# Kernel optimization log

Hardware: AMD Instinct MI355X
Metric: run time of the kernel (lower is better)

## Reference

```python
import jax, jax.numpy as jnp
import numpy as np

H = 300          # hidden_size
M = 256          # molecules
L = 128          # atoms per molecule (uniform -> pad/unpad is a reshape)
A = 1 + M * L    # atoms incl. zero-padding row 0
NB = 6           # max neighbor bonds per atom
B = 1 + 4 * M * L  # directed bonds incl. zero-padding row 0
ATOM_FDIM = 133
BOND_FDIM = 147
DEPTH = 3


def _lin(key, out_d, in_d):
    return (jax.random.normal(key, (out_d, in_d), jnp.float32) / np.sqrt(in_d)).astype(jnp.float32)


def setup_inputs() -> dict:
    key = jax.random.key(0)
    ks = jax.random.split(key, 24)
    s = 1.0 / np.sqrt(H)
    return {
        "f_atoms": jax.random.normal(ks[0], (A, ATOM_FDIM), jnp.float32),
        "f_bonds": jax.random.normal(ks[1], (B, BOND_FDIM), jnp.float32),
        "a2b": jax.random.randint(ks[2], (A, NB), 0, B),
        "b2a": jax.random.randint(ks[3], (B,), 0, A),
        "b2revb": jax.random.randint(ks[4], (B,), 0, B),
        "W_i_atom": _lin(ks[5], H, ATOM_FDIM),
        "W_i_bond": _lin(ks[6], H, BOND_FDIM),
        "W_h0": _lin(ks[7], H, H),
        "W_h1": _lin(ks[8], H, H),
        "W_lr": _lin(ks[9], H, 3 * H),
        "gru_bias": jax.random.uniform(ks[10], (H,), jnp.float32, -s, s),
        "Wih_f": _lin(ks[11], 3 * H, H),
        "Whh_f": _lin(ks[12], 3 * H, H),
        "bih_f": jax.random.uniform(ks[13], (3 * H,), jnp.float32, -s, s),
        "bhh_f": jax.random.uniform(ks[14], (3 * H,), jnp.float32, -s, s),
        "Wih_b": _lin(ks[15], 3 * H, H),
        "Whh_b": _lin(ks[16], 3 * H, H),
        "bih_b": jax.random.uniform(ks[17], (3 * H,), jnp.float32, -s, s),
        "bhh_b": jax.random.uniform(ks[18], (3 * H,), jnp.float32, -s, s),
        "W_o": _lin(ks[19], H, 2 * H),
        "b_o": jax.random.uniform(ks[20], (H,), jnp.float32, -s, s),
    }


def _gru_dir(x, h0, Wih, Whh, bih, bhh, reverse):
    # x: [M, T, H], h0: [M, H] -> outputs [M, T, H], torch.nn.GRU gate math
    gi_all = jnp.swapaxes(x, 0, 1) @ Wih.T + bih  # [T, M, 3H]

    def step(h, gi):
        gh = h @ Whh.T + bhh
        ir, iz, inn = jnp.split(gi, 3, axis=-1)
        hr, hz, hn = jnp.split(gh, 3, axis=-1)
        r = jax.nn.sigmoid(ir + hr)
        z = jax.nn.sigmoid(iz + hz)
        n = jnp.tanh(inn + r * hn)
        h_new = (1.0 - z) * n + z * h
        return h_new, h_new

    _, ys = jax.lax.scan(step, h0, gi_all, reverse=reverse)
    return jnp.swapaxes(ys, 0, 1)


def reference(f_atoms, f_bonds, a2b, b2a, b2revb, W_i_atom, W_i_bond, W_h0, W_h1,
              W_lr, gru_bias, Wih_f, Whh_f, bih_f, bhh_f, Wih_b, Whh_b, bih_b, bhh_b,
              W_o, b_o):
    relu = jax.nn.relu
    input_atom = relu(f_atoms @ W_i_atom.T)            # [A, H]
    message_atom = input_atom
    input_bond = relu(f_bonds @ W_i_bond.T)            # [B, H]
    message_bond = input_bond

    W_h = [W_h0, W_h1]
    for d in range(DEPTH - 1):
        nei = message_bond[a2b]                        # [A, NB, H] gather
        agg = nei.sum(axis=1) * nei.max(axis=1)        # sum * max aggregation
        message_atom = message_atom + agg
        rev = message_bond[b2revb]                     # [B, H]
        message_bond = message_atom[b2a] - rev
        message_bond = message_bond @ W_h[d].T
        message_bond = relu(input_bond + message_bond)  # dropout p=0

    nei = message_bond[a2b]
    agg = nei.sum(axis=1) * nei.max(axis=1)
    node = jnp.concatenate([agg, message_atom, input_atom], axis=1) @ W_lr.T  # [A, H]

    # BatchGRU: uniform molecule sizes -> pad/unpad is a reshape
    message = relu(node + gru_bias)                    # [A, H]
    msg = message[1:].reshape(M, L, H)
    hid = node[1:].reshape(M, L, H)
    h0 = hid.max(axis=1)                               # [M, H] per-mol max init state
    out_f = _gru_dir(msg, h0, Wih_f, Whh_f, bih_f, bhh_f, reverse=False)
    out_b = _gru_dir(msg, h0, Wih_b, Whh_b, bih_b, bhh_b, reverse=True)
    gru_out = jnp.concatenate([out_f, out_b], axis=-1).reshape(M * L, 2 * H)
    row0 = jnp.concatenate([message[0:1], message[0:1]], axis=1)
    agg2 = jnp.concatenate([row0, gru_out], axis=0)    # [A, 2H]

    atom_hiddens = relu(agg2 @ W_o.T + b_o)            # [A, H]
    mol_vecs = atom_hiddens[1:].reshape(M, L, H).mean(axis=1)  # [M, H]
    return mol_vecs
```

## Files before the change

kernel.cpp:

```cpp
#include <hip/hip_runtime.h>
#include <math.h>

#define HH   300
#define H3   900
#define MMOL 256
#define LATM 128
#define AA   32769
#define NBB  6
#define BBND 131073
#define AFD  133
#define BFD  147
#define MLR  (MMOL * LATM)

static __device__ __forceinline__ float sigm(float x) { return 1.0f / (1.0f + expf(-x)); }

template<bool RELU, bool BIAS, bool ACCUM>
__global__ __launch_bounds__(256)
void gemm_big(const float* __restrict__ X, int ldx, const float* __restrict__ W, int ldw,
              const float* __restrict__ Bias, float* __restrict__ C,
              int rows, int N, int K)
{
    __shared__ float Xs[16][132];
    __shared__ float Ws[16][68];
    const int row0 = blockIdx.x * 128;
    const int col0 = blockIdx.y * 64;
    const int tid  = threadIdx.x;
    const int tm   = (tid >> 4) * 8;
    const int tn   = (tid & 15) * 4;
    const bool xv  = ((ldx & 3) == 0);
    const bool wv  = ((ldw & 3) == 0);

    float acc[8][4];
#pragma unroll
    for (int i = 0; i < 8; ++i)
#pragma unroll
        for (int j = 0; j < 4; ++j) acc[i][j] = 0.0f;

    for (int k0 = 0; k0 < K; k0 += 16) {
        const int rem = K - k0;
#pragma unroll
        for (int l = 0; l < 2; ++l) {
            int s = tid + l * 256;
            int r = s >> 2, kq = (s & 3) * 4;
            int gr = row0 + r;
            float v0 = 0, v1 = 0, v2 = 0, v3 = 0;
            if (gr < rows) {
                const float* xp = X + (long)gr * ldx + k0 + kq;
                if (xv && rem >= 16) {
                    float4 t4 = *(const float4*)xp;
                    v0 = t4.x; v1 = t4.y; v2 = t4.z; v3 = t4.w;
                } else {
                    if (kq + 0 < rem) v0 = xp[0];
                    if (kq + 1 < rem) v1 = xp[1];
                    if (kq + 2 < rem) v2 = xp[2];
                    if (kq + 3 < rem) v3 = xp[3];
                }
            }
            Xs[kq + 0][r] = v0; Xs[kq + 1][r] = v1;
            Xs[kq + 2][r] = v2; Xs[kq + 3][r] = v3;
        }
        {
            int r = tid >> 2, kq = (tid & 3) * 4;
            int gc = col0 + r;
            float v0 = 0, v1 = 0, v2 = 0, v3 = 0;
            if (gc < N) {
                const float* wp = W + (long)gc * ldw + k0 + kq;
                if (wv && rem >= 16) {
                    float4 t4 = *(const float4*)wp;
                    v0 = t4.x; v1 = t4.y; v2 = t4.z; v3 = t4.w;
                } else {
                    if (kq + 0 < rem) v0 = wp[0];
                    if (kq + 1 < rem) v1 = wp[1];
                    if (kq + 2 < rem) v2 = wp[2];
                    if (kq + 3 < rem) v3 = wp[3];
                }
            }
            Ws[kq + 0][r] = v0; Ws[kq + 1][r] = v1;
            Ws[kq + 2][r] = v2; Ws[kq + 3][r] = v3;
        }
        __syncthreads();
#pragma unroll
        for (int kk = 0; kk < 16; ++kk) {
            float4 xa = *(const float4*)&Xs[kk][tm];
            float4 xb = *(const float4*)&Xs[kk][tm + 4];
            float4 wq = *(const float4*)&Ws[kk][tn];
            float xr[8] = {xa.x, xa.y, xa.z, xa.w, xb.x, xb.y, xb.z, xb.w};
            float wr[4] = {wq.x, wq.y, wq.z, wq.w};
#pragma unroll
            for (int i = 0; i < 8; ++i)
#pragma unroll
                for (int j = 0; j < 4; ++j)
                    acc[i][j] += xr[i] * wr[j];
        }
        __syncthreads();
    }

#pragma unroll
    for (int i = 0; i < 8; ++i) {
        int gr = row0 + tm + i;
        if (gr >= rows) continue;
#pragma unroll
        for (int j = 0; j < 4; ++j) {
            int gc = col0 + tn + j;
            if (gc >= N) continue;
            float v = acc[i][j];
            if (BIAS)  v += Bias[gc];
            if (ACCUM) v += C[(long)gr * N + gc];
            if (RELU)  v = fmaxf(v, 0.0f);
            C[(long)gr * N + gc] = v;
        }
    }
}

__global__ void transpose_kernel(const float* __restrict__ in, float* __restrict__ out,
                                 int N, int K)
{
    long idx = (long)blockIdx.x * blockDim.x + threadIdx.x;
    if (idx >= (long)N * K) return;
    int k = (int)(idx / N), n = (int)(idx - (long)k * N);
    out[idx] = in[(long)n * K + k];
}

__global__ __launch_bounds__(256)
void vw_hi_gemm(float* __restrict__ P, const float* __restrict__ W, int rows)
{
    __shared__ float Xs[16][132];
    __shared__ float Ws[16][192];
    const int row0 = blockIdx.x * 128;
    const int tid  = threadIdx.x;
    const int tm   = (tid >> 4) * 8;
    const int tn   = (tid & 15) * 4;

    float acc[8][12];
#pragma unroll
    for (int i = 0; i < 8; ++i)
#pragma unroll
        for (int j = 0; j < 12; ++j) acc[i][j] = 0.0f;

    for (int k0 = 0; k0 < 300; k0 += 16) {
        const int rem = 300 - k0;
#pragma unroll
        for (int l = 0; l < 2; ++l) {
            int s = tid + l * 256;
            int r = s >> 2, kq = (s & 3) * 4;
            int gr = row0 + r;
            float v0 = 0, v1 = 0, v2 = 0, v3 = 0;
            if (gr < rows) {
                const float* xp = P + (long)gr * 300 + k0 + kq;
                if (rem >= 16) {
                    float4 t4 = *(const float4*)xp;
                    v0 = t4.x; v1 = t4.y; v2 = t4.z; v3 = t4.w;
                } else {
                    if (kq + 0 < rem) v0 = xp[0];
                    if (kq + 1 < rem) v1 = xp[1];
                    if (kq + 2 < rem) v2 = xp[2];
                    if (kq + 3 < rem) v3 = xp[3];
                }
            }
            Xs[kq + 0][r] = v0; Xs[kq + 1][r] = v1;
            Xs[kq + 2][r] = v2; Xs[kq + 3][r] = v3;
        }
        for (int s = tid; s < 600; s += 256) {
            int r = s >> 2, kq = (s & 3) * 4;
            const float* wp = W + (long)(150 + r) * 300 + k0 + kq;
            float v0 = 0, v1 = 0, v2 = 0, v3 = 0;
            if (rem >= 16) {
                float4 t4 = *(const float4*)wp;
                v0 = t4.x; v1 = t4.y; v2 = t4.z; v3 = t4.w;
            } else {
                if (kq + 0 < rem) v0 = wp[0];
                if (kq + 1 < rem) v1 = wp[1];
                if (kq + 2 < rem) v2 = wp[2];
                if (kq + 3 < rem) v3 = wp[3];
            }
            Ws[kq + 0][r] = v0; Ws[kq + 1][r] = v1;
            Ws[kq + 2][r] = v2; Ws[kq + 3][r] = v3;
        }
        __syncthreads();
#pragma unroll
        for (int kk = 0; kk < 16; ++kk) {
            float4 xa = *(const float4*)&Xs[kk][tm];
            float4 xb = *(const float4*)&Xs[kk][tm + 4];
            float4 w0 = *(const float4*)&Ws[kk][tn];
            float4 w1 = *(const float4*)&Ws[kk][tn + 64];
            float4 w2 = *(const float4*)&Ws[kk][tn + 128];
            float xr[8] = {xa.x, xa.y, xa.z, xa.w, xb.x, xb.y, xb.z, xb.w};
            float wr[12] = {w0.x, w0.y, w0.z, w0.w, w1.x, w1.y, w1.z, w1.w,
                            w2.x, w2.y, w2.z, w2.w};
#pragma unroll
            for (int i = 0; i < 8; ++i)
#pragma unroll
                for (int j = 0; j < 12; ++j)
                    acc[i][j] += xr[i] * wr[j];
        }
        __syncthreads();
    }

#pragma unroll
    for (int i = 0; i < 8; ++i) {
        int gr = row0 + tm + i;
        if (gr >= rows) continue;
#pragma unroll
        for (int c = 0; c < 3; ++c)
#pragma unroll
            for (int j = 0; j < 4; ++j) {
                int cn = tn + c * 64 + j;
                if (cn < 150) P[(long)gr * 300 + cn] = acc[i][c * 4 + j];
            }
    }
}

__global__ __launch_bounds__(256)
void bond_half(const float* __restrict__ FB, const float* __restrict__ WiB,
               const float* __restrict__ Th, const float* __restrict__ Vsrc, int vstride,
               const int* __restrict__ b2a, const int* __restrict__ b2revb,
               float* __restrict__ P, int c0, int rows)
{
    __shared__ float Xs[16][132];
    __shared__ float Ws[16][68];
    __shared__ int ra[128], rb[128];
    const int row0 = blockIdx.x * 128;
    const int col0 = blockIdx.y * 64;
    const int tid  = threadIdx.x;

    if (tid < 128) {
        int gr = row0 + tid;
        ra[tid] = (gr < rows) ? b2a[gr] : 0;
    } else {
        int m = tid - 128;
        int gr = row0 + m;
        rb[m] = (gr < rows) ? b2revb[gr] : 0;
    }

    const int tm = (tid >> 4) * 8;
    const int tn = (tid & 15) * 4;
    float acc[8][4];
#pragma unroll
    for (int i = 0; i < 8; ++i)
#pragma unroll
        for (int j = 0; j < 4; ++j) acc[i][j] = 0.0f;

    for (int k0 = 0; k0 < BFD; k0 += 16) {
        const int rem = BFD - k0;
#pragma unroll
        for (int l = 0; l < 2; ++l) {
            int s = tid + l * 256;
            int r = s >> 2, kq = (s & 3) * 4;
            int gr = row0 + r;
            float v0 = 0, v1 = 0, v2 = 0, v3 = 0;
            if (gr < rows) {
                const float* xp = FB + (long)gr * BFD + k0 + kq;
                if (kq + 0 < rem) v0 = xp[0];
                if (kq + 1 < rem) v1 = xp[1];
                if (kq + 2 < rem) v2 = xp[2];
                if (kq + 3 < rem) v3 = xp[3];
            }
            Xs[kq + 0][r] = v0; Xs[kq + 1][r] = v1;
            Xs[kq + 2][r] = v2; Xs[kq + 3][r] = v3;
        }
        {
            int r = tid >> 2, kq = (tid & 3) * 4;
            int gc = col0 + r;
            float v0 = 0, v1 = 0, v2 = 0, v3 = 0;
            if (gc < 150) {
                const float* wp = WiB + (long)(c0 + gc) * BFD + k0 + kq;
                if (kq + 0 < rem) v0 = wp[0];
                if (kq + 1 < rem) v1 = wp[1];
                if (kq + 2 < rem) v2 = wp[2];
                if (kq + 3 < rem) v3 = wp[3];
            }
            Ws[kq + 0][r] = v0; Ws[kq + 1][r] = v1;
            Ws[kq + 2][r] = v2; Ws[kq + 3][r] = v3;
        }
        __syncthreads();
#pragma unroll
        for (int kk = 0; kk < 16; ++kk) {
            float4 xa = *(const float4*)&Xs[kk][tm];
            float4 xb = *(const float4*)&Xs[kk][tm + 4];
            float4 wq = *(const float4*)&Ws[kk][tn];
            float xr[8] = {xa.x, xa.y, xa.z, xa.w, xb.x, xb.y, xb.z, xb.w};
            float wr[4] = {wq.x, wq.y, wq.z, wq.w};
#pragma unroll
            for (int i = 0; i < 8; ++i)
#pragma unroll
                for (int j = 0; j < 4; ++j)
                    acc[i][j] += xr[i] * wr[j];
        }
        __syncthreads();
    }

#pragma unroll
    for (int i = 0; i < 8; ++i) {
        int gr = row0 + tm + i;
        if (gr >= rows) continue;
        int a  = ra[tm + i];
        int rv = rb[tm + i];
#pragma unroll
        for (int j = 0; j < 4; ++j) {
            int cn = col0 + tn + j;
            if (cn >= 150) continue;
            float ib = fmaxf(acc[i][j], 0.0f);
            float v  = ib + Th[(long)a * 150 + cn] - Vsrc[(long)rv * vstride + cn];
            P[(long)gr * 300 + c0 + cn] = fmaxf(v, 0.0f);
        }
    }
}

template<bool ADD>
__global__ void aggregate(const float* __restrict__ mb, const int* __restrict__ a2b,
                          float* __restrict__ dst)
{
    long idx = (long)blockIdx.x * blockDim.x + threadIdx.x;
    if (idx >= (long)AA * HH) return;
    int a = (int)(idx / HH);
    int h = (int)(idx - (long)a * HH);
    const int* nb = a2b + (long)a * NBB;
    float s = 0.0f, mx = -INFINITY;
#pragma unroll
    for (int i = 0; i < NBB; ++i) {
        float v = mb[(long)nb[i] * HH + h];
        s += v;
        mx = fmaxf(mx, v);
    }
    float r = s * mx;
    if (ADD) r += dst[idx];
    dst[idx] = r;
}

__global__ void msgx_kernel(const float* __restrict__ node, const float* __restrict__ gbias,
                            float* __restrict__ msgx)
{
    long idx = (long)blockIdx.x * blockDim.x + threadIdx.x;
    if (idx >= (long)MLR * HH) return;
    int h = (int)(idx % HH);
    msgx[idx] = fmaxf(node[idx + HH] + gbias[h], 0.0f);
}

__global__ void h0_kernel(const float* __restrict__ node, float* __restrict__ hf)
{
    int idx = blockIdx.x * blockDim.x + threadIdx.x;
    if (idx >= MMOL * HH) return;
    int m = idx / HH;
    int h = idx - m * HH;
    long base = (long)(1 + m * LATM) * HH + h;
    float mx = -INFINITY;
    for (int t = 0; t < LATM; ++t) mx = fmaxf(mx, node[base + (long)t * HH]);
    hf[idx] = mx;
}

__global__ __launch_bounds__(1024)
void gru_scan3(const float* __restrict__ WhhT_f, const float* __restrict__ bhh_f,
               const float* __restrict__ WhhT_b, const float* __restrict__ bhh_b,
               const float* __restrict__ h0, float* __restrict__ gi_f,
               float* __restrict__ gi_b)
{
    const int bid  = blockIdx.x;
    const int xcd  = bid & 7;
    const int dir  = (xcd >= 4) ? 1 : 0;
    const int rank = (bid >> 3) * 4 + (xcd & 3);
    const int m0   = rank * 2;
    const float* WhhT = dir ? WhhT_b : WhhT_f;
    const float* bhh  = dir ? bhh_b  : bhh_f;
    float*       gi   = dir ? gi_b   : gi_f;
    const int tid = threadIdx.x;

    __shared__ float hs[2][304];
    __shared__ float ghs[2][H3];

    float bb = (tid < H3) ? bhh[tid] : 0.0f;

    for (int i = tid; i < 150; i += 1024) {
        int mm = i / 75, q = (i - mm * 75) * 4;
        *(float4*)&hs[mm][q] = *(const float4*)&h0[(long)(m0 + mm) * HH + q];
    }
    __syncthreads();

    for (int s = 0; s < LATM; ++s) {
        const int t = dir ? (LATM - 1 - s) : s;

        if (tid < H3) {
            float a0 = 0.0f, a1 = 0.0f;
            const float* wh = WhhT + tid;
#pragma unroll 4
            for (int k0 = 0; k0 < HH; k0 += 4) {
                float w0 = wh[(long)(k0 + 0) * H3];
                float w1 = wh[(long)(k0 + 1) * H3];
                float w2 = wh[(long)(k0 + 2) * H3];
                float w3 = wh[(long)(k0 + 3) * H3];
                float4 h0v = *(const float4*)&hs[0][k0];
                float4 h1v = *(const float4*)&hs[1][k0];
                a0 += h0v.x * w0 + h0v.y * w1 + h0v.z * w2 + h0v.w * w3;
                a1 += h1v.x * w0 + h1v.y * w1 + h1v.z * w2 + h1v.w * w3;
            }
            ghs[0][tid] = a0 + bb;
            ghs[1][tid] = a1 + bb;
        }
        __syncthreads();

        if (tid < 2 * HH) {
            int mm = tid / HH, hh = tid - mm * HH;
            long row = (long)(m0 + mm) * LATM + t;
            float* g = gi + row * H3;
            float ir = g[hh], iz = g[HH + hh], inn = g[2 * HH + hh];
            float r  = sigm(ir + ghs[mm][hh]);
            float z  = sigm(iz + ghs[mm][HH + hh]);
            float nn = tanhf(inn + r * ghs[mm][2 * HH + hh]);
            float hn = (1.0f - z) * nn + z * hs[mm][hh];
            hs[mm][hh] = hn;
            g[hh] = hn;
        }
        __syncthreads();
    }
}

__global__ void mean_kernel(const float* __restrict__ ah, float* __restrict__ out)
{
    int idx = blockIdx.x * blockDim.x + threadIdx.x;
    if (idx >= MMOL * HH) return;
    int m = idx / HH;
    int j = idx - m * HH;
    long base = (long)m * LATM * HH + j;
    float s = 0.0f;
    for (int t = 0; t < LATM; ++t) s += ah[base + (long)t * HH];
    out[idx] = s * (1.0f / LATM);
}

static inline int cdiv(long a, long b) { return (int)((a + b - 1) / b); }

extern "C" void kernel_launch(void* const* d_in, const int* in_sizes, int n_in,
                              void* d_out, int out_size, void* d_ws, size_t ws_size,
                              hipStream_t stream)
{
    const float* f_atoms  = (const float*)d_in[0];
    const float* f_bonds  = (const float*)d_in[1];
    const int*   a2b      = (const int*)d_in[2];
    const int*   b2a      = (const int*)d_in[3];
    const int*   b2revb   = (const int*)d_in[4];
    const float* W_i_atom = (const float*)d_in[5];
    const float* W_i_bond = (const float*)d_in[6];
    const float* W_h0     = (const float*)d_in[7];
    const float* W_h1     = (const float*)d_in[8];
    const float* W_lr     = (const float*)d_in[9];
    const float* gru_bias = (const float*)d_in[10];
    const float* Wih_f    = (const float*)d_in[11];
    const float* Whh_f    = (const float*)d_in[12];
    const float* bih_f    = (const float*)d_in[13];
    const float* bhh_f    = (const float*)d_in[14];
    const float* Wih_b    = (const float*)d_in[15];
    const float* Whh_b    = (const float*)d_in[16];
    const float* bih_b    = (const float*)d_in[17];
    const float* bhh_b    = (const float*)d_in[18];
    const float* W_o      = (const float*)d_in[19];
    const float* b_o      = (const float*)d_in[20];
    float* out = (float*)d_out;

    const size_t NEED = 295530016;
    if (ws_size < NEED) return;

    char* b = (char*)d_ws;
    float* P   = (float*)b;
    float* S   = (float*)(b + 157287600);
    float* MA  = (float*)(b + 235931408);
    float* TH  = (float*)(b + 275254208);

    float* Pia  = P + (size_t)AA * HH;
    float* giF  = (float*)b;
    float* giB  = (float*)(b + 117964800);
    float* MSGX = MA;
    float* AH   = MA;
    float* H0   = TH;
    float* WhhT_f = TH + 76800;
    float* WhhT_b = TH + 346800;

    dim3 blk(256);
    const int gA = cdiv((long)AA * HH, 256);
    dim3 gmA (cdiv(AA, 128),   cdiv(HH, 64));
    dim3 gmB3(cdiv(BBND, 128), cdiv(HH, 64));
    dim3 gmB1(cdiv(BBND, 128), cdiv(150, 64));
    dim3 gmT (cdiv(AA, 128),   cdiv(150, 64));
    dim3 gmG (cdiv(MLR, 128),  cdiv(H3, 64));
    dim3 gmO (cdiv(MLR, 128),  cdiv(HH, 64));

    gemm_big<true, false, false><<<gmA, blk, 0, stream>>>(
        f_atoms, AFD, W_i_atom, AFD, nullptr, MA, AA, HH, AFD);
    gemm_big<true, false, false><<<gmB3, blk, 0, stream>>>(
        f_bonds, BFD, W_i_bond, BFD, nullptr, P, BBND, HH, BFD);

    const float* Wh[2] = { W_h0, W_h1 };
    for (int d = 0; d < 2; ++d) {
        const float* W = Wh[d];
        aggregate<true><<<gA, blk, 0, stream>>>(P, a2b, MA);
        gemm_big<false, false, false><<<gmB1, blk, 0, stream>>>(
            P, HH, W, HH, nullptr, S, BBND, 150, HH);
        vw_hi_gemm<<<cdiv(BBND, 128), blk, 0, stream>>>(P, W, BBND);
        gemm_big<false, false, false><<<gmT, blk, 0, stream>>>(
            MA, HH, W + 150 * HH, HH, nullptr, TH, AA, 150, HH);
        bond_half<<<gmB1, blk, 0, stream>>>(
            f_bonds, W_i_bond, TH, P, 300, b2a, b2revb, P, 150, BBND);
        gemm_big<false, false, false><<<gmT, blk, 0, stream>>>(
            MA, HH, W, HH, nullptr, TH, AA, 150, HH);
        bond_half<<<gmB1, blk, 0, stream>>>(
            f_bonds, W_i_bond, TH, S, 150, b2a, b2revb, P, 0, BBND);
    }

    aggregate<false><<<gA, blk, 0, stream>>>(P, a2b, S);

    gemm_big<true, false, false><<<gmA, blk, 0, stream>>>(
        f_atoms, AFD, W_i_atom, AFD, nullptr, Pia, AA, HH, AFD);
    gemm_big<false, false, false><<<gmA, blk, 0, stream>>>(
        S,   HH, W_lr,          H3, nullptr, P, AA, HH, HH);
    gemm_big<false, false, true><<<gmA, blk, 0, stream>>>(
        MA,  HH, W_lr + HH,     H3, nullptr, P, AA, HH, HH);
    gemm_big<false, false, true><<<gmA, blk, 0, stream>>>(
        Pia, HH, W_lr + 2 * HH, H3, nullptr, P, AA, HH, HH);

    msgx_kernel<<<cdiv((long)MLR * HH, 256), blk, 0, stream>>>(P, gru_bias, MSGX);
    h0_kernel<<<cdiv(MMOL * HH, 256), blk, 0, stream>>>(P, H0);
    transpose_kernel<<<cdiv(270000, 256), blk, 0, stream>>>(Whh_f, WhhT_f, H3, HH);
    transpose_kernel<<<cdiv(270000, 256), blk, 0, stream>>>(Whh_b, WhhT_b, H3, HH);

    gemm_big<false, true, false><<<gmG, blk, 0, stream>>>(
        MSGX, HH, Wih_f, HH, bih_f, giF, MLR, H3, HH);
    gemm_big<false, true, false><<<gmG, blk, 0, stream>>>(
        MSGX, HH, Wih_b, HH, bih_b, giB, MLR, H3, HH);

    gru_scan3<<<dim3(256), dim3(1024), 0, stream>>>(
        WhhT_f, bhh_f, WhhT_b, bhh_b, H0, giF, giB);

    gemm_big<false, false, false><<<gmO, blk, 0, stream>>>(
        giF, H3, W_o,      2 * HH, nullptr, AH, MLR, HH, HH);
    gemm_big<true, true, true><<<gmO, blk, 0, stream>>>(
        giB, H3, W_o + HH, 2 * HH, b_o,     AH, MLR, HH, HH);

    mean_kernel<<<cdiv(MMOL * HH, 256), blk, 0, stream>>>(AH, out);
}
```

Before: 5.624 ms.

## Register-prefetch next GEMM tile and vectorize GRU recurrent weight loads

The generic tiled GEMM now loads the next K-tile from global memory into registers while the current shared-memory tile is being computed, so load latency overlaps with FMA work. Separately, the recurrent weights Whh are repacked into groups of four consecutive k-values per output, so the GRU scan can fetch them with one float4 load instead of four strided scalar loads. The prefetch costs extra registers in the GEMM and may lower occupancy, and the repack kernel hardcodes the 900x300 shape.

```diff
diff --git a/kernel.cpp b/kernel.cpp
--- a/kernel.cpp
+++ b/kernel.cpp
@@ -30,13 +30,9 @@
     const bool xv  = ((ldx & 3) == 0);
     const bool wv  = ((ldw & 3) == 0);
 
-    float acc[8][4];
-#pragma unroll
-    for (int i = 0; i < 8; ++i)
-#pragma unroll
-        for (int j = 0; j < 4; ++j) acc[i][j] = 0.0f;
-
-    for (int k0 = 0; k0 < K; k0 += 16) {
+    float px[2][4], pw[4];
+
+    auto loadTile = [&](int k0) {
         const int rem = K - k0;
 #pragma unroll
         for (int l = 0; l < 2; ++l) {
@@ -56,8 +52,7 @@
                     if (kq + 3 < rem) v3 = xp[3];
                 }
             }
-            Xs[kq + 0][r] = v0; Xs[kq + 1][r] = v1;
-            Xs[kq + 2][r] = v2; Xs[kq + 3][r] = v3;
+            px[l][0] = v0; px[l][1] = v1; px[l][2] = v2; px[l][3] = v3;
         }
         {
             int r = tid >> 2, kq = (tid & 3) * 4;
@@ -75,10 +70,35 @@
                     if (kq + 3 < rem) v3 = wp[3];
                 }
             }
-            Ws[kq + 0][r] = v0; Ws[kq + 1][r] = v1;
-            Ws[kq + 2][r] = v2; Ws[kq + 3][r] = v3;
-        }
-        __syncthreads();
+            pw[0] = v0; pw[1] = v1; pw[2] = v2; pw[3] = v3;
+        }
+    };
+    auto commitTile = [&]() {
+#pragma unroll
+        for (int l = 0; l < 2; ++l) {
+            int s = tid + l * 256;
+            int r = s >> 2, kq = (s & 3) * 4;
+            Xs[kq + 0][r] = px[l][0]; Xs[kq + 1][r] = px[l][1];
+            Xs[kq + 2][r] = px[l][2]; Xs[kq + 3][r] = px[l][3];
+        }
+        {
+            int r = tid >> 2, kq = (tid & 3) * 4;
+            Ws[kq + 0][r] = pw[0]; Ws[kq + 1][r] = pw[1];
+            Ws[kq + 2][r] = pw[2]; Ws[kq + 3][r] = pw[3];
+        }
+    };
+
+    float acc[8][4];
+#pragma unroll
+    for (int i = 0; i < 8; ++i)
+#pragma unroll
+        for (int j = 0; j < 4; ++j) acc[i][j] = 0.0f;
+
+    loadTile(0);
+    for (int k0 = 0; k0 < K; k0 += 16) {
+        commitTile();
+        __syncthreads();
+        if (k0 + 16 < K) loadTile(k0 + 16);
 #pragma unroll
         for (int kk = 0; kk < 16; ++kk) {
             float4 xa = *(const float4*)&Xs[kk][tm];
@@ -112,13 +132,12 @@
     }
 }
 
-__global__ void transpose_kernel(const float* __restrict__ in, float* __restrict__ out,
-                                 int N, int K)
+__global__ void transposeQ(const float* __restrict__ in, float* __restrict__ out)
 {
     long idx = (long)blockIdx.x * blockDim.x + threadIdx.x;
-    if (idx >= (long)N * K) return;
-    int k = (int)(idx / N), n = (int)(idx - (long)k * N);
-    out[idx] = in[(long)n * K + k];
+    if (idx >= 270000) return;
+    int n = (int)(idx / 300), k = (int)(idx - (long)n * 300);
+    out[(long)(k >> 2) * 3600 + n * 4 + (k & 3)] = in[idx];
 }
 
 __global__ __launch_bounds__(256)
@@ -349,8 +368,8 @@
 }
 
 __global__ __launch_bounds__(1024)
-void gru_scan3(const float* __restrict__ WhhT_f, const float* __restrict__ bhh_f,
-               const float* __restrict__ WhhT_b, const float* __restrict__ bhh_b,
+void gru_scan3(const float* __restrict__ WQ_f, const float* __restrict__ bhh_f,
+               const float* __restrict__ WQ_b, const float* __restrict__ bhh_b,
                const float* __restrict__ h0, float* __restrict__ gi_f,
                float* __restrict__ gi_b)
 {
@@ -359,9 +378,9 @@
     const int dir  = (xcd >= 4) ? 1 : 0;
     const int rank = (bid >> 3) * 4 + (xcd & 3);
     const int m0   = rank * 2;
-    const float* WhhT = dir ? WhhT_b : WhhT_f;
-    const float* bhh  = dir ? bhh_b  : bhh_f;
-    float*       gi   = dir ? gi_b   : gi_f;
+    const float* WQ  = dir ? WQ_b  : WQ_f;
+    const float* bhh = dir ? bhh_b : bhh_f;
+    float*       gi  = dir ? gi_b  : gi_f;
     const int tid = threadIdx.x;
 
     __shared__ float hs[2][304];
@@ -380,17 +399,15 @@
 
         if (tid < H3) {
             float a0 = 0.0f, a1 = 0.0f;
-            const float* wh = WhhT + tid;
+            const float* wq = WQ + (long)tid * 4;
 #pragma unroll 4
             for (int k0 = 0; k0 < HH; k0 += 4) {
-                float w0 = wh[(long)(k0 + 0) * H3];
-                float w1 = wh[(long)(k0 + 1) * H3];
-                float w2 = wh[(long)(k0 + 2) * H3];
-                float w3 = wh[(long)(k0 + 3) * H3];
+                float4 w = *(const float4*)wq;
+                wq += 3600;
                 float4 h0v = *(const float4*)&hs[0][k0];
                 float4 h1v = *(const float4*)&hs[1][k0];
-                a0 += h0v.x * w0 + h0v.y * w1 + h0v.z * w2 + h0v.w * w3;
-                a1 += h1v.x * w0 + h1v.y * w1 + h1v.z * w2 + h1v.w * w3;
+                a0 += h0v.x * w.x + h0v.y * w.y + h0v.z * w.z + h0v.w * w.w;
+                a1 += h1v.x * w.x + h1v.y * w.y + h1v.z * w.z + h1v.w * w.w;
             }
             ghs[0][tid] = a0 + bb;
             ghs[1][tid] = a1 + bb;
@@ -469,8 +486,8 @@
     float* MSGX = MA;
     float* AH   = MA;
     float* H0   = TH;
-    float* WhhT_f = TH + 76800;
-    float* WhhT_b = TH + 346800;
+    float* WQ_f = TH + 76800;
+    float* WQ_b = TH + 346800;
 
     dim3 blk(256);
     const int gA = cdiv((long)AA * HH, 256);
@@ -516,8 +533,8 @@
 
     msgx_kernel<<<cdiv((long)MLR * HH, 256), blk, 0, stream>>>(P, gru_bias, MSGX);
     h0_kernel<<<cdiv(MMOL * HH, 256), blk, 0, stream>>>(P, H0);
-    transpose_kernel<<<cdiv(270000, 256), blk, 0, stream>>>(Whh_f, WhhT_f, H3, HH);
-    transpose_kernel<<<cdiv(270000, 256), blk, 0, stream>>>(Whh_b, WhhT_b, H3, HH);
+    transposeQ<<<cdiv(270000, 256), blk, 0, stream>>>(Whh_f, WQ_f);
+    transposeQ<<<cdiv(270000, 256), blk, 0, stream>>>(Whh_b, WQ_b);
 
     gemm_big<false, true, false><<<gmG, blk, 0, stream>>>(
         MSGX, HH, Wih_f, HH, bih_f, giF, MLR, H3, HH);
@@ -525,7 +542,7 @@
         MSGX, HH, Wih_b, HH, bih_b, giB, MLR, H3, HH);
 
     gru_scan3<<<dim3(256), dim3(1024), 0, stream>>>(
-        WhhT_f, bhh_f, WhhT_b, bhh_b, H0, giF, giB);
+        WQ_f, bhh_f, WQ_b, bhh_b, H0, giF, giB);
 
     gemm_big<false, false, false><<<gmO, blk, 0, stream>>>(
         giF, H3, W_o,      2 * HH, nullptr, AH, MLR, HH, HH);
```

After: 5.206 ms. -7.4%, faster.
